# Performance work log

Measured on AMD Instinct MI355X. Metric: run time of the kernel, lower is better.

Reference implementation:

```python
import jax, jax.numpy as jnp
import numpy as np

EPS = 1e-7
NUM_ROUTINGS = 3


def squash(s):
    # s: [..., V]; maps norm into [0, 1)
    norm = jnp.linalg.norm(s, axis=-1, keepdims=True)
    coef = norm ** 2 / (norm ** 2 + 1.0)
    return coef * s / (norm + EPS)


def setup_inputs() -> dict:
    key = jax.random.key(0)
    k1, k2 = jax.random.split(key)
    B, N, Q = 32, 32768, 8          # batch, num_primary, dim_primary
    D, V = 10, 16                   # num_digit, dim_digit
    primary_caps = jax.random.normal(k1, (B, N, Q), dtype=jnp.float32)
    # glorot-ish scale for W [num_digit, num_primary, dim_digit, dim_primary]
    W = jax.random.normal(k2, (D, N, V, Q), dtype=jnp.float32) * (1.0 / np.sqrt(Q))
    return {"primary_caps": primary_caps, "W": W}


def reference(primary_caps, W):
    # u_hat[b,d,n,v] = sum_q W[d,n,v,q] * u[b,n,q]  -> [B, D, N, V]
    u_hat = jnp.einsum("dnvq,bnq->bdnv", W, primary_caps)
    B, D, N, V = u_hat.shape
    b = jnp.zeros((B, D, N), dtype=u_hat.dtype)
    v = None
    for r in range(NUM_ROUTINGS):
        c = jax.nn.softmax(b, axis=1)                      # softmax over digit axis
        s = jnp.einsum("bdn,bdnv->bdv", c, u_hat)          # [B, D, V]
        v = squash(s)                                      # [B, D, V]
        if r < NUM_ROUTINGS - 1:
            b = b + jnp.einsum("bdnv,bdv->bdn", u_hat, v)  # agreement update
    return v  # [B, num_digit, dim_digit]
```

## Files before the change

### kernel.cpp

```cpp
#include <hip/hip_runtime.h>

namespace {
constexpr int kB = 32;
constexpr int kN = 32768;
constexpr int kQ = 8;
constexpr int kD = 10;
constexpr int kV = 16;
constexpr int kRows = kB * kD;
constexpr int kNT = 4;
constexpr int kTiles = kN / kNT;
constexpr int kThreads = 512;
constexpr int kGrid = 512;
constexpr int kWBlk = 576;
constexpr int kWReg = 23552;
constexpr int kUReg = kNT * kB * 32;
constexpr int kBuf = kWReg + kUReg;
}

__device__ __forceinline__ void g2lds16(const void* g, void* l) {
  __builtin_amdgcn_global_load_lds(
      (const __attribute__((address_space(1))) unsigned int*)g,
      (__attribute__((address_space(3))) unsigned int*)l, 16, 0, 0);
}

template <int CTRL>
__device__ __forceinline__ float dpp_mv(float x) {
  return __int_as_float(__builtin_amdgcn_update_dpp(
      0, __float_as_int(x), CTRL, 0xF, 0xF, true));
}

__device__ __forceinline__ void stage_tile(const float* __restrict__ u,
                                           const float* __restrict__ W,
                                           char* buf, int n0) {
  const int wv = threadIdx.x >> 6;
  const int ln = threadIdx.x & 63;
  #pragma unroll
  for (int k = 0; k < 4; ++k) {
    const int s = wv + 8 * k;
    if (s < 23) {
      const int g = s * 64 + ln;
      const int blk = g / 36;
      const int c = g - blk * 36;
      const char* src;
      if (g < 1440 && c < 32) {
        const int n_l = blk / 10, d = blk - n_l * 10;
        const int qh = c >> 4, v = c & 15;
        src = (const char*)W + ((size_t)d * kN + n0 + n_l) * 512 +
              (size_t)(v * 32 + qh * 16);
      } else {
        src = (const char*)W;
      }
      g2lds16(src, buf + s * 1024);
    } else if (s < 27) {
      const int s2 = s - 23;
      const int h = s2 * 64 + ln;
      const int n_l = h >> 6, r = h & 63, b = r >> 1, qh = r & 1;
      const char* src = (const char*)u +
          ((size_t)b * kN + n0 + n_l) * 32 + (size_t)qh * 16;
      g2lds16(src, buf + kWReg + s2 * 1024);
    }
  }
}

template <int PHASE>
__launch_bounds__(kThreads, 2)
__global__ void routing_pass(const float* __restrict__ u,
                             const float* __restrict__ W,
                             const float* __restrict__ vprev,
                             float* __restrict__ s_out) {
  __shared__ __align__(16) char smem[2 * kBuf];
  const int t = threadIdx.x;
  const int bgrp = t >> 6;
  const int ln = t & 63;
  const int dslot = ln >> 2;
  const int vq = ln & 3;
  const bool act = (dslot < kD);
  const int dd = act ? dslot : dslot - kD;
  const int b0 = bgrp * 4;

  float vp[4][4];
  if constexpr (PHASE != 0) {
    #pragma unroll
    for (int bb = 0; bb < 4; ++bb)
      #pragma unroll
      for (int j = 0; j < 4; ++j)
        vp[bb][j] = vprev[((b0 + bb) * kD + dd) * kV + j * 4 + vq];
  }

  float acc[4][4];
  #pragma unroll
  for (int bb = 0; bb < 4; ++bb)
    #pragma unroll
    for (int j = 0; j < 4; ++j) acc[bb][j] = 0.0f;

  int tile = blockIdx.x;
  int cur = 0;
  stage_tile(u, W, smem, tile * kNT);

  for (; tile < kTiles; tile += kGrid) {
    __syncthreads();
    const int nxt = tile + kGrid;
    if (nxt < kTiles)
      stage_tile(u, W, smem + (cur ^ 1) * kBuf, nxt * kNT);

    const char* base = smem + cur * kBuf;
    #pragma unroll
    for (int nl = 0; nl < kNT; ++nl) {
      float uh[4][4];
      #pragma unroll
      for (int bb = 0; bb < 4; ++bb)
        #pragma unroll
        for (int j = 0; j < 4; ++j) uh[bb][j] = 0.0f;
      const char* wb = base + (nl * kD + dd) * kWBlk + vq * 16;
      const char* ub = base + kWReg + nl * 1024 + b0 * 32;
      #pragma unroll
      for (int qh = 0; qh < 2; ++qh) {
        float uu[4][4];
        #pragma unroll
        for (int bb = 0; bb < 4; ++bb) {
          const float4 a = *(const float4*)(ub + bb * 32 + qh * 16);
          uu[bb][0] = a.x; uu[bb][1] = a.y; uu[bb][2] = a.z; uu[bb][3] = a.w;
        }
        #pragma unroll
        for (int j = 0; j < 4; ++j) {
          const float4 w4 = *(const float4*)(wb + qh * 256 + j * 64);
          #pragma unroll
          for (int bb = 0; bb < 4; ++bb) {
            uh[bb][j] = fmaf(w4.x, uu[bb][0], uh[bb][j]);
            uh[bb][j] = fmaf(w4.y, uu[bb][1], uh[bb][j]);
            uh[bb][j] = fmaf(w4.z, uu[bb][2], uh[bb][j]);
            uh[bb][j] = fmaf(w4.w, uu[bb][3], uh[bb][j]);
          }
        }
      }
      #pragma unroll
      for (int bb = 0; bb < 4; ++bb) {
        float c;
        if constexpr (PHASE != 0) {
          float lg = uh[bb][0] * vp[bb][0];
          lg = fmaf(uh[bb][1], vp[bb][1], lg);
          lg = fmaf(uh[bb][2], vp[bb][2], lg);
          lg = fmaf(uh[bb][3], vp[bb][3], lg);
          lg += dpp_mv<0xB1>(lg);
          lg += dpp_mv<0x4E>(lg);
          const float e = act ? __expf(lg) : 0.0f;
          float den = e;
          den += dpp_mv<0x124>(den);
          den += dpp_mv<0x128>(den);
          den += __shfl_xor(den, 16);
          den += __shfl_xor(den, 32);
          c = e * __builtin_amdgcn_rcpf(den);
        } else {
          c = 1.0f;
        }
        #pragma unroll
        for (int j = 0; j < 4; ++j) acc[bb][j] = fmaf(c, uh[bb][j], acc[bb][j]);
      }
    }
    cur ^= 1;
  }

  if (act) {
    const float scale = (PHASE == 0) ? 0.1f : 1.0f;
    #pragma unroll
    for (int bb = 0; bb < 4; ++bb) {
      float* srow = s_out + ((b0 + bb) * kD + dslot) * kV + vq;
      #pragma unroll
      for (int j = 0; j < 4; ++j)
        atomicAdd(&srow[j * 4], acc[bb][j] * scale);
    }
  }
}

template <int MODE>
__global__ void squash_kernel(float* __restrict__ s,
                              float* __restrict__ vprev,
                              float* __restrict__ out) {
  const int t = threadIdx.x;
  if (t >= kRows) return;
  float* sr = s + t * kV;
  float sv[kV];
  float n2 = 0.0f;
  #pragma unroll
  for (int v = 0; v < kV; ++v) {
    sv[v] = sr[v];
    n2 = fmaf(sv[v], sv[v], n2);
  }
  if (MODE != 2) {
    #pragma unroll
    for (int v = 0; v < kV; ++v) sr[v] = 0.0f;
  }
  const float norm = sqrtf(n2);
  const float coef = n2 / ((n2 + 1.0f) * (norm + 1e-7f));
  float* dst = (MODE == 2) ? (out + t * kV) : (vprev + t * kV);
  #pragma unroll
  for (int v = 0; v < kV; ++v) {
    float val = coef * sv[v];
    if (MODE == 1) val += dst[v];
    dst[v] = val;
  }
}

extern "C" void kernel_launch(void* const* d_in, const int* in_sizes, int n_in,
                              void* d_out, int out_size, void* d_ws, size_t ws_size,
                              hipStream_t stream) {
  const float* u = reinterpret_cast<const float*>(d_in[0]);
  const float* W = reinterpret_cast<const float*>(d_in[1]);
  float* out = reinterpret_cast<float*>(d_out);

  float* s = reinterpret_cast<float*>(d_ws);
  float* vprev = s + kRows * kV;
  const size_t sbytes = (size_t)kRows * kV * sizeof(float);

  (void)hipMemsetAsync(s, 0, sbytes, stream);
  routing_pass<0><<<kGrid, kThreads, 0, stream>>>(u, W, nullptr, s);
  squash_kernel<0><<<1, kThreads, 0, stream>>>(s, vprev, out);

  routing_pass<1><<<kGrid, kThreads, 0, stream>>>(u, W, vprev, s);
  squash_kernel<1><<<1, kThreads, 0, stream>>>(s, vprev, out);

  routing_pass<1><<<kGrid, kThreads, 0, stream>>>(u, W, vprev, s);
  squash_kernel<2><<<1, kThreads, 0, stream>>>(s, vprev, out);
}
```

Measured before the change: 569.5 us.

## Load u directly as wave-uniform scalar loads and batch softmax over four batches

```diff
diff --git a/kernel.cpp b/kernel.cpp
--- a/kernel.cpp
+++ b/kernel.cpp
@@ -13,8 +13,7 @@
 constexpr int kGrid = 512;
 constexpr int kWBlk = 576;
 constexpr int kWReg = 23552;
-constexpr int kUReg = kNT * kB * 32;
-constexpr int kBuf = kWReg + kUReg;
+constexpr int kBuf = kWReg;
 }
 
 __device__ __forceinline__ void g2lds16(const void* g, void* l) {
@@ -29,13 +28,12 @@
       0, __float_as_int(x), CTRL, 0xF, 0xF, true));
 }
 
-__device__ __forceinline__ void stage_tile(const float* __restrict__ u,
-                                           const float* __restrict__ W,
+__device__ __forceinline__ void stage_tile(const float* __restrict__ W,
                                            char* buf, int n0) {
   const int wv = threadIdx.x >> 6;
   const int ln = threadIdx.x & 63;
   #pragma unroll
-  for (int k = 0; k < 4; ++k) {
+  for (int k = 0; k < 3; ++k) {
     const int s = wv + 8 * k;
     if (s < 23) {
       const int g = s * 64 + ln;
@@ -51,13 +49,6 @@
         src = (const char*)W;
       }
       g2lds16(src, buf + s * 1024);
-    } else if (s < 27) {
-      const int s2 = s - 23;
-      const int h = s2 * 64 + ln;
-      const int n_l = h >> 6, r = h & 63, b = r >> 1, qh = r & 1;
-      const char* src = (const char*)u +
-          ((size_t)b * kN + n0 + n_l) * 32 + (size_t)qh * 16;
-      g2lds16(src, buf + kWReg + s2 * 1024);
     }
   }
 }
@@ -70,7 +61,7 @@
                              float* __restrict__ s_out) {
   __shared__ __align__(16) char smem[2 * kBuf];
   const int t = threadIdx.x;
-  const int bgrp = t >> 6;
+  const int bgrp = __builtin_amdgcn_readfirstlane(t >> 6);
   const int ln = t & 63;
   const int dslot = ln >> 2;
   const int vq = ln & 3;
@@ -95,30 +86,31 @@
 
   int tile = blockIdx.x;
   int cur = 0;
-  stage_tile(u, W, smem, tile * kNT);
+  stage_tile(W, smem, tile * kNT);
 
   for (; tile < kTiles; tile += kGrid) {
     __syncthreads();
     const int nxt = tile + kGrid;
     if (nxt < kTiles)
-      stage_tile(u, W, smem + (cur ^ 1) * kBuf, nxt * kNT);
+      stage_tile(W, smem + (cur ^ 1) * kBuf, nxt * kNT);
 
     const char* base = smem + cur * kBuf;
     #pragma unroll
     for (int nl = 0; nl < kNT; ++nl) {
+      const int n = tile * kNT + nl;
       float uh[4][4];
       #pragma unroll
       for (int bb = 0; bb < 4; ++bb)
         #pragma unroll
         for (int j = 0; j < 4; ++j) uh[bb][j] = 0.0f;
       const char* wb = base + (nl * kD + dd) * kWBlk + vq * 16;
-      const char* ub = base + kWReg + nl * 1024 + b0 * 32;
       #pragma unroll
       for (int qh = 0; qh < 2; ++qh) {
         float uu[4][4];
         #pragma unroll
         for (int bb = 0; bb < 4; ++bb) {
-          const float4 a = *(const float4*)(ub + bb * 32 + qh * 16);
+          const float4 a = *(const float4*)(
+              u + ((size_t)(b0 + bb) * kN + n) * kQ + qh * 4);
           uu[bb][0] = a.x; uu[bb][1] = a.y; uu[bb][2] = a.z; uu[bb][3] = a.w;
         }
         #pragma unroll
@@ -133,28 +125,40 @@
           }
         }
       }
-      #pragma unroll
-      for (int bb = 0; bb < 4; ++bb) {
-        float c;
-        if constexpr (PHASE != 0) {
-          float lg = uh[bb][0] * vp[bb][0];
-          lg = fmaf(uh[bb][1], vp[bb][1], lg);
-          lg = fmaf(uh[bb][2], vp[bb][2], lg);
-          lg = fmaf(uh[bb][3], vp[bb][3], lg);
-          lg += dpp_mv<0xB1>(lg);
-          lg += dpp_mv<0x4E>(lg);
-          const float e = act ? __expf(lg) : 0.0f;
-          float den = e;
-          den += dpp_mv<0x124>(den);
-          den += dpp_mv<0x128>(den);
-          den += __shfl_xor(den, 16);
-          den += __shfl_xor(den, 32);
-          c = e * __builtin_amdgcn_rcpf(den);
-        } else {
-          c = 1.0f;
+      if constexpr (PHASE != 0) {
+        float lg[4];
+        #pragma unroll
+        for (int bb = 0; bb < 4; ++bb) {
+          float t0 = uh[bb][0] * vp[bb][0];
+          t0 = fmaf(uh[bb][1], vp[bb][1], t0);
+          t0 = fmaf(uh[bb][2], vp[bb][2], t0);
+          t0 = fmaf(uh[bb][3], vp[bb][3], t0);
+          t0 += dpp_mv<0xB1>(t0);
+          t0 += dpp_mv<0x4E>(t0);
+          lg[bb] = t0;
         }
-        #pragma unroll
-        for (int j = 0; j < 4; ++j) acc[bb][j] = fmaf(c, uh[bb][j], acc[bb][j]);
+        const float ta = (vq & 2) ? lg[2] : lg[0];
+        const float tb = (vq & 2) ? lg[3] : lg[1];
+        const float lsel = (vq & 1) ? tb : ta;
+        const float esel = act ? __expf(lsel) : 0.0f;
+        float den = esel;
+        den += dpp_mv<0x124>(den);
+        den += dpp_mv<0x128>(den);
+        den += __shfl_xor(den, 16);
+        den += __shfl_xor(den, 32);
+        const float csel = esel * __builtin_amdgcn_rcpf(den);
+        const float cb[4] = {dpp_mv<0x00>(csel), dpp_mv<0x55>(csel),
+                             dpp_mv<0xAA>(csel), dpp_mv<0xFF>(csel)};
+        #pragma unroll
+        for (int bb = 0; bb < 4; ++bb)
+          #pragma unroll
+          for (int j = 0; j < 4; ++j)
+            acc[bb][j] = fmaf(cb[bb], uh[bb][j], acc[bb][j]);
+      } else {
+        #pragma unroll
+        for (int bb = 0; bb < 4; ++bb)
+          #pragma unroll
+          for (int j = 0; j < 4; ++j) acc[bb][j] += uh[bb][j];
       }
     }
     cur ^= 1;
```

New measurement: 795.3 us. 39.6% more time.
